# Kernel optimization log

Hardware: AMD Instinct MI355X
Metric: run time of the kernel (lower is better)

## Reference

```python
import jax, jax.numpy as jnp
import numpy as np

N_PRED = 10000
N_GT = 1000
NUM_CLASSES = 80
IMG_H = 800
IMG_W = 1333
EPS = 1e-12
ALPHA, GAMMA, CLS_W = 0.25, 2.0, 2.0
L1_W, IOU_W = 5.0, 2.0
CENTER_RADIUS = 2.5
CAND_TOPK = 5


def _make_boxes(key, n, w, h):
    k1, k2 = jax.random.split(key)
    cxcy = jax.random.uniform(k1, (n, 2)) * jnp.array([w, h], jnp.float32)
    wh = jax.random.uniform(k2, (n, 2)) * 190.0 + 10.0
    return jnp.concatenate([cxcy - wh / 2, cxcy + wh / 2], axis=1).astype(jnp.float32)


def setup_inputs() -> dict:
    key = jax.random.key(0)
    k1, k2, k3, k4 = jax.random.split(key, 4)
    return {
        'pred_logits': jax.random.normal(k1, (N_PRED, NUM_CLASSES), jnp.float32),
        'pred_boxes': _make_boxes(k2, N_PRED, IMG_W, IMG_H),
        'gt_bboxes': _make_boxes(k3, N_GT, IMG_W, IMG_H),
        'gt_labels': jax.random.randint(k4, (N_GT,), 0, NUM_CLASSES),
        'img_h': IMG_H,
        'img_w': IMG_W,
    }


def _pairwise_iou_giou(pred, gt):
    area_p = (pred[:, 2] - pred[:, 0]) * (pred[:, 3] - pred[:, 1])
    area_g = (gt[:, 2] - gt[:, 0]) * (gt[:, 3] - gt[:, 1])
    lt = jnp.maximum(pred[:, None, :2], gt[None, :, :2])
    rb = jnp.minimum(pred[:, None, 2:], gt[None, :, 2:])
    wh = jnp.clip(rb - lt, 0.0)
    inter = wh[..., 0] * wh[..., 1]                       # [N,G]
    union = area_p[:, None] + area_g[None, :] - inter
    iou = inter / jnp.maximum(union, EPS)
    elt = jnp.minimum(pred[:, None, :2], gt[None, :, :2])
    erb = jnp.maximum(pred[:, None, 2:], gt[None, :, 2:])
    ewh = jnp.clip(erb - elt, 0.0)
    enclose = ewh[..., 0] * ewh[..., 1]
    giou = iou - (enclose - union) / jnp.maximum(enclose, EPS)
    return iou, giou


def _center_info(pred, gt):
    # pred/gt in xyxy; uses pred box centers, strict inequalities as in source
    pcx = (pred[:, 0] + pred[:, 2]) * 0.5
    pcy = (pred[:, 1] + pred[:, 3]) * 0.5
    gx1, gy1, gx2, gy2 = gt[:, 0], gt[:, 1], gt[:, 2], gt[:, 3]
    in_boxes = ((pcx[:, None] > gx1) & (pcx[:, None] < gx2) &
                (pcy[:, None] > gy1) & (pcy[:, None] < gy2))
    gcx, gcy = (gx1 + gx2) * 0.5, (gy1 + gy2) * 0.5
    gw, gh = gx2 - gx1, gy2 - gy1
    r = CENTER_RADIUS
    in_centers = ((pcx[:, None] > gcx - r * gw) & (pcx[:, None] < gcx + r * gw) &
                  (pcy[:, None] > gcy - r * gh) & (pcy[:, None] < gcy + r * gh))
    valid = in_boxes.any(1) | in_centers.any(1)
    return valid, in_boxes & in_centers


def _compute_cost_and_ious(pred_logits, pred_boxes, gt_bboxes, gt_labels, img_h, img_w):
    # FocalLossCost
    p = jax.nn.sigmoid(pred_logits)
    neg = -jnp.log1p(-(p - EPS)) * (1 - ALPHA) * p ** GAMMA
    pos = -jnp.log(p + EPS) * ALPHA * (1 - p) ** GAMMA
    cls_cost = (pos - neg)[:, gt_labels] * CLS_W            # [N,G]
    # BBoxL1Cost (normalized by image size)
    factor = jnp.array([img_w, img_h, img_w, img_h], jnp.float32)
    l1_cost = jnp.sum(jnp.abs(pred_boxes[:, None, :] / factor -
                              gt_bboxes[None, :, :] / factor), -1) * L1_W
    # IoUCost (giou) + pairwise ious for dynamic-k
    ious, giou = _pairwise_iou_giou(pred_boxes, gt_bboxes)
    iou_cost = -giou * IOU_W
    valid_mask, in_boxes_and_center = _center_info(pred_boxes, gt_bboxes)
    cost = cls_cost + l1_cost + iou_cost + jnp.where(in_boxes_and_center, 0.0, 100.0)
    cost = cost + jnp.where(valid_mask, 0.0, 10000.0)[:, None]
    return cost, ious


def _dynamic_k_matching(cost, ious):
    n, g = cost.shape
    k = min(CAND_TOPK, n)
    topk_ious, _ = jax.lax.top_k(ious.T, k)                 # [G,k]
    dynamic_ks = jnp.maximum(topk_ious.sum(1).astype(jnp.int32), 1)
    _, idx = jax.lax.top_k(-cost.T, k)                      # [G,k] smallest costs per gt
    vals = (jnp.arange(k)[None, :] < dynamic_ks[:, None]).astype(cost.dtype)
    cols = jnp.broadcast_to(jnp.arange(g)[:, None], (g, k))
    mm = jnp.zeros_like(cost).at[idx, cols].max(vals)       # scatter 1s per gt column
    # resolve priors matched to >1 gt (note: mask is reused stale inside the loop, as in source)
    prior_mask = mm.sum(1) > 1
    cmin = jnp.argmin(cost, axis=1)
    mm = jnp.where(prior_mask[:, None], jax.nn.one_hot(cmin, g, dtype=cost.dtype), mm)

    def cond(state):
        m, _ = state
        return jnp.any(m.sum(0) == 0)

    def body(state):
        m, c = state
        matched_q = m.sum(1) > 0
        c = c + 100000.0 * matched_q[:, None].astype(c.dtype)
        unmatched = m.sum(0) == 0
        pos = jnp.argmin(c, axis=0)                         # [G]
        oh = jax.nn.one_hot(pos, n, dtype=c.dtype).T        # [N,G]
        m = jnp.where(unmatched[None, :], oh, m)
        cmin2 = jnp.argmin(c, axis=1)
        m_fix = jnp.where(prior_mask[:, None], jax.nn.one_hot(cmin2, g, dtype=c.dtype), m)
        m = jnp.where(jnp.any(m.sum(1) > 1), m_fix, m)
        return (m, c)

    mm, _ = jax.lax.while_loop(cond, body, (mm, cost))
    fg_mask = mm.sum(1) > 0
    matched = jnp.argmax(mm, axis=1).astype(jnp.int32)
    return fg_mask, jnp.where(fg_mask, matched, 0)


def reference(pred_logits, pred_boxes, gt_bboxes, gt_labels, img_h, img_w):
    cost, ious = _compute_cost_and_ious(pred_logits, pred_boxes, gt_bboxes,
                                        gt_labels, img_h, img_w)
    fg_mask, matched_gt = _dynamic_k_matching(cost, ious)
    # dense form: matched_gt[i] valid only where fg_mask[i] (fixed-shape version of
    # the original's compressed matched_gt_inds = mm[fg_mask].argmax(1))
    return fg_mask, matched_gt
```

## Files before the change

### kernel.cpp

```cpp
#include <hip/hip_runtime.h>
#include <cfloat>
#include <cmath>

#define NP 10000
#define NG 1000
#define NC 80
#define LMAX 6
#define NCH 4
#define CHSZ (NP / NCH)
#define WMAIN 39
#define WTAIL 4

#define RI_BIG  0x3fffffff
#define KMAX    0xFFFFFFFFFFFFFFFFull

#define TKEY    0xC248000000000000ull

#define WCAP    768

#define PSLOTS  2560
#define PCAP    2560
#define FCAP    1024

__device__ __forceinline__ bool lexless(float av, int ai, float bv, int bi) {
    return (av < bv) || (av == bv && ai < bi);
}

__device__ __forceinline__ unsigned long long packkey(float v, int idx) {
    unsigned u = __float_as_uint(v);
    u ^= (unsigned)(((int)u) >> 31) | 0x80000000u;
    return ((unsigned long long)u << 32) | (unsigned)idx;
}
__device__ __forceinline__ int keyidx(unsigned long long k) {
    return (int)(unsigned)(k & 0xFFFFFFFFu);
}

__device__ __forceinline__ float inflate(float c, int k) {
    for (int q = 0; q < k; q++) c += 100000.0f;
    return c;
}

__device__ __forceinline__ void cost_iou(float4 p, float4 pn, float4 pi,
        float4 g, float4 cb, float4 Gn, float ga, float clsv,
        float& cc_out, float& iou_out) {
#pragma clang fp contract(off)
    float wx = fminf(p.z, g.z) - fmaxf(p.x, g.x); wx = fmaxf(wx, 0.0f);
    float wy = fminf(p.w, g.w) - fmaxf(p.y, g.y); wy = fmaxf(wy, 0.0f);
    float inter = wx * wy;
    float uni = pi.z + ga - inter;
    float iou = inter / fmaxf(uni, 1e-12f);
    float ex = fmaxf(p.z, g.z) - fminf(p.x, g.x); ex = fmaxf(ex, 0.0f);
    float ey = fmaxf(p.w, g.w) - fminf(p.y, g.y); ey = fmaxf(ey, 0.0f);
    float enc = ex * ey;
    float giou = iou - (enc - uni) / fmaxf(enc, 1e-12f);
    float l1 = ((fabsf(pn.x - Gn.x) + fabsf(pn.y - Gn.y))
                + fabsf(pn.z - Gn.z)) + fabsf(pn.w - Gn.w);
    float cc = clsv + l1 * 5.0f;
    cc = cc + (-giou * 2.0f);
    bool inb = (pi.x > g.x && pi.x < g.z && pi.y > g.y && pi.y < g.w);
    bool inc = (pi.x > cb.x && pi.x < cb.z && pi.y > cb.y && pi.y < cb.w);
    cc = cc + ((inb && inc) ? 0.0f : 100.0f);
    cc = cc + pi.w;
    cc_out = cc; iou_out = iou;
}

__device__ __forceinline__ void ins5k(unsigned long long* kv,
        unsigned long long key) {
    if (key < kv[4]) {
        kv[4] = key;
#pragma unroll
        for (int t = 4; t > 0; t--)
            if (kv[t] < kv[t-1]) { unsigned long long tv = kv[t]; kv[t] = kv[t-1]; kv[t-1] = tv; }
    }
}
__device__ __forceinline__ void ins5i(float* iv, float iou) {
    if (iou > iv[4]) {
        iv[4] = iou;
#pragma unroll
        for (int t = 4; t > 0; t--)
            if (iv[t] > iv[t-1]) { float tv = iv[t]; iv[t] = iv[t-1]; iv[t-1] = tv; }
    }
}

__device__ __forceinline__ void cswapk(unsigned long long& a,
        unsigned long long& b) {
    unsigned long long lo = (a < b) ? a : b;
    unsigned long long hi = (a < b) ? b : a;
    a = lo; b = hi;
}
__device__ __forceinline__ void sort5k(unsigned long long* a) {
    cswapk(a[0],a[1]); cswapk(a[3],a[4]); cswapk(a[2],a[4]);
    cswapk(a[2],a[3]); cswapk(a[1],a[4]); cswapk(a[0],a[3]);
    cswapk(a[0],a[2]); cswapk(a[1],a[3]); cswapk(a[1],a[2]);
}
__device__ __forceinline__ void cswapi(float& a, float& b) {
    float hi = fmaxf(a, b), lo = fminf(a, b);
    a = hi; b = lo;
}
__device__ __forceinline__ void sort5i(float* a) {
    cswapi(a[0],a[1]); cswapi(a[3],a[4]); cswapi(a[2],a[4]);
    cswapi(a[2],a[3]); cswapi(a[1],a[4]); cswapi(a[0],a[3]);
    cswapi(a[0],a[2]); cswapi(a[1],a[3]); cswapi(a[1],a[2]);
}

__device__ __forceinline__ void wavemerge5(unsigned long long* kv, float* iv) {
#pragma unroll
    for (int d = 1; d < 64; d <<= 1) {
        unsigned long long r0 = __shfl_xor(kv[0], d);
        unsigned long long r1 = __shfl_xor(kv[1], d);
        unsigned long long r2 = __shfl_xor(kv[2], d);
        unsigned long long r3 = __shfl_xor(kv[3], d);
        unsigned long long r4 = __shfl_xor(kv[4], d);
        kv[0] = (kv[0] < r4) ? kv[0] : r4;
        kv[1] = (kv[1] < r3) ? kv[1] : r3;
        kv[2] = (kv[2] < r2) ? kv[2] : r2;
        kv[3] = (kv[3] < r1) ? kv[3] : r1;
        kv[4] = (kv[4] < r0) ? kv[4] : r0;
        sort5k(kv);
        float s0 = __shfl_xor(iv[0], d);
        float s1 = __shfl_xor(iv[1], d);
        float s2 = __shfl_xor(iv[2], d);
        float s3 = __shfl_xor(iv[3], d);
        float s4 = __shfl_xor(iv[4], d);
        iv[0] = fmaxf(iv[0], s4);
        iv[1] = fmaxf(iv[1], s3);
        iv[2] = fmaxf(iv[2], s2);
        iv[3] = fmaxf(iv[3], s1);
        iv[4] = fmaxf(iv[4], s0);
        sort5i(iv);
    }
}

__device__ __forceinline__ void wavered_lex(float& best, int& bi) {
#pragma unroll
    for (int d = 1; d < 64; d <<= 1) {
        float ov = __shfl_xor(best, d);
        int oi = __shfl_xor(bi, d);
        if (lexless(ov, oi, best, bi)) { best = ov; bi = oi; }
    }
}

#define CLS_TI 64
#define PB_CLS0 40
#define PB_G0   197
#define PB_V0   201
#define PB_SORT 2701
__global__ __launch_bounds__(256) void k_prep(const float* __restrict__ logits,
        const float* __restrict__ pb, const float* __restrict__ gb,
        const int* __restrict__ glab,
        const int* __restrict__ imgw, const int* __restrict__ imgh,
        float* __restrict__ clsval, float4* __restrict__ pnorm,
        float4* __restrict__ pinfo, float4* __restrict__ gcb,
        float4* __restrict__ gnm, float* __restrict__ gar,
        int* rowcnt, int* rowfirst, int* rowiter, int* prior, int* priorcol,
        int* colsum, int* scal, int* priorslot, int* gorder)
{
    __shared__ float sl[CLS_TI * (NC + 1)];
    int b = blockIdx.x;
    if (b == PB_SORT) {
        __shared__ int hist[NC];
        __shared__ int basec[NC];
        int tid = threadIdx.x;
        if (tid < NC) hist[tid] = 0;
        __syncthreads();
        for (int j = tid; j < NG; j += 256) atomicAdd(&hist[glab[j]], 1);
        __syncthreads();
        if (tid == 0) {
            int acc = 0;
            for (int c = 0; c < NC; c++) { basec[c] = acc; acc += hist[c]; }
        }
        __syncthreads();
        for (int j = tid; j < NG; j += 256) {
            int pos = atomicAdd(&basec[glab[j]], 1);
            gorder[pos] = j;
        }
        return;
    }
    if (b < PB_CLS0) {
        int i = b * 256 + threadIdx.x;
        if (i < NP) {
            rowcnt[i] = 0; rowfirst[i] = 0x7fffffff; rowiter[i] = RI_BIG;
            prior[i] = 0; priorcol[i] = 0; priorslot[i] = -1;
        }
        if (i < NG) colsum[i] = 0;
        if (i < 32) scal[i] = 0;
    } else if (b < PB_G0) {
        int i0 = (b - PB_CLS0) * CLS_TI;
        bool full = (i0 + CLS_TI) <= NP;
        if (full) {
            const float* src = logits + (size_t)i0 * NC;
            for (int e = threadIdx.x; e < CLS_TI * NC; e += 256) {
                int di = e / NC, c = e - di * NC;
                sl[di * (NC + 1) + c] = src[e];
            }
        } else {
            for (int e = threadIdx.x; e < CLS_TI * NC; e += 256) {
                int di = e / NC, c = e - di * NC;
                int i = i0 + di;
                sl[di * (NC + 1) + c] = (i < NP) ? logits[(size_t)i * NC + c] : 0.0f;
            }
        }
        __syncthreads();
        for (int e = threadIdx.x; e < CLS_TI * NC; e += 256) {
            int c = e >> 6, di = e & 63;
            int i = i0 + di;
            if (i >= NP) continue;
            float x = sl[di * (NC + 1) + c];
            float p = 1.0f / (1.0f + expf(-x));
            float neg = -log1pf(-(p - 1e-12f)) * 0.75f * (p * p);
            float om = 1.0f - p;
            float pos = -logf(p + 1e-12f) * 0.25f * (om * om);
            clsval[(size_t)c * NP + i] = (pos - neg) * 2.0f;
        }
    } else if (b < PB_V0) {
#pragma clang fp contract(off)
        int j = (b - PB_G0) * 256 + threadIdx.x;
        if (j < NG) {
            float fw = (float)imgw[0], fh = (float)imgh[0];
            float4 g = ((const float4*)gb)[j];
            float gcx = (g.x + g.z) * 0.5f, gcy = (g.y + g.w) * 0.5f;
            float gw = g.z - g.x, gh = g.w - g.y;
            float4 cb; cb.x = gcx - 2.5f * gw; cb.y = gcy - 2.5f * gh;
            cb.z = gcx + 2.5f * gw; cb.w = gcy + 2.5f * gh;
            gcb[j] = cb;
            float4 Gn; Gn.x = g.x / fw; Gn.y = g.y / fh; Gn.z = g.z / fw; Gn.w = g.w / fh;
            gnm[j] = Gn;
            gar[j] = (g.z - g.x) * (g.w - g.y);
        }
    } else {
#pragma clang fp contract(off)
        int wave = threadIdx.x >> 6;
        int lane = threadIdx.x & 63;
        int i = (b - PB_V0) * 4 + wave;
        if (i >= NP) return;
        float4 p = ((const float4*)pb)[i];
        float pcx = (p.x + p.z) * 0.5f, pcy = (p.y + p.w) * 0.5f;
        int vb = 0, vc = 0;
        const float4* gb4 = (const float4*)gb;
        for (int jb = 0; jb < NG; jb += 64) {
            int j = jb + lane;
            if (j < NG) {
                float4 g = gb4[j];
                vb |= (pcx > g.x && pcx < g.z && pcy > g.y && pcy < g.w) ? 1 : 0;
                float gcx = (g.x + g.z) * 0.5f, gcy = (g.y + g.w) * 0.5f;
                float gw = g.z - g.x, gh = g.w - g.y;
                vc |= (pcx > gcx - 2.5f * gw && pcx < gcx + 2.5f * gw &&
                       pcy > gcy - 2.5f * gh && pcy < gcy + 2.5f * gh) ? 1 : 0;
            }
            if (__any(vb | vc)) break;
        }
        int any = __any(vb | vc) ? 1 : 0;
        if (lane == 0) {
            float fw = (float)imgw[0], fh = (float)imgh[0];
            float4 pn; pn.x = p.x / fw; pn.y = p.y / fh; pn.z = p.z / fw; pn.w = p.w / fh;
            pnorm[i] = pn;
            float4 pi4; pi4.x = pcx; pi4.y = pcy;
            pi4.z = (p.z - p.x) * (p.w - p.y);
            pi4.w = any ? 0.0f : 10000.0f;
            pinfo[i] = pi4;
        }
    }
}

__global__ __launch_bounds__(256) void k_cost2(
        const float* __restrict__ pb, const float* __restrict__ gb,
        const int* __restrict__ glab, const float* __restrict__ clsval,
        const float4* __restrict__ pnorm, const float4* __restrict__ pinfo,
        const float4* __restrict__ gcb, const float4* __restrict__ gnm,
        const float* __restrict__ gar, const int* __restrict__ gorder,
        int* __restrict__ rowcnt, int* __restrict__ rowfirst,
        int* __restrict__ rowiter, int* __restrict__ top5,
        int* __restrict__ dkarr)
{
    __shared__ int s_list[4 * WCAP];
    __shared__ unsigned long long s_k4[4][5];
    __shared__ float s_iv4[4][5];
    __shared__ int s_redo;

    int bb = blockIdx.x;
    int j = gorder[(bb & 7) * (NG / 8) + (bb >> 3)];
    int tid = threadIdx.x;
    int wid = tid >> 6;
    int ln  = tid & 63;
    float4 g  = ((const float4*)gb)[j];
    float4 cb = gcb[j];
    float4 Gn = gnm[j];
    float  ga = gar[j];
    const float* clscol = clsval + (size_t)glab[j] * NP;
    const float4* pb4 = (const float4*)pb;
    int base_i = wid * CHSZ;

    int wbase = 0;
    for (int k = 0; k <= WMAIN; k++) {
        bool valid = (k < WMAIN) | (ln < WTAIL);
        int i = base_i + ln + k * 64;
        float4 p = pb4[valid ? i : base_i];
        bool o = valid & (p.z > g.x) & (g.z > p.x) & (p.w > g.y) & (g.w > p.y);
        unsigned long long m = __ballot(o ? 1 : 0);
        if (o) {
            int slot = wbase + __popcll(m & ((1ull << ln) - 1ull));
            if (slot < WCAP) s_list[wid * WCAP + slot] = i;
        }
        wbase += __popcll(m);
    }
    int cnt = wbase;
    bool overflow = (cnt > WCAP);

    unsigned long long kv[5]; float iv[5];
#pragma unroll
    for (int t = 0; t < 5; t++) { kv[t] = KMAX; iv[t] = overflow ? -1.0f : 0.0f; }

    if (!overflow) {
        for (int q = ln; q < cnt; q += 64) {
            int i = s_list[wid * WCAP + q];
            float cc, iou;
            cost_iou(pb4[i], pnorm[i], pinfo[i], g, cb, Gn, ga, clscol[i], cc, iou);
            ins5k(kv, packkey(cc, i)); ins5i(iv, iou);
        }
    } else {
        for (int k = 0; k <= WMAIN; k++) {
            bool valid = (k < WMAIN) | (ln < WTAIL);
            if (valid) {
                int i = base_i + ln + k * 64;
                float cc, iou;
                cost_iou(pb4[i], pnorm[i], pinfo[i], g, cb, Gn, ga, clscol[i], cc, iou);
                ins5k(kv, packkey(cc, i)); ins5i(iv, iou);
            }
        }
    }
    wavemerge5(kv, iv);

    if (ln == 0) {
#pragma unroll
        for (int t = 0; t < 5; t++) { s_k4[wid][t] = kv[t]; s_iv4[wid][t] = iv[t]; }
    }
    __syncthreads();

    unsigned long long mk0=KMAX, mk1=KMAX, mk2=KMAX, mk3=KMAX, mk4=KMAX;
    float mi0=-2.0f, mi1=-2.0f, mi2=-2.0f, mi3=-2.0f, mi4=-2.0f;
    if (tid == 0) {
        int h0 = 0, h1 = 0, h2 = 0, h3 = 0;
        unsigned long long mk[5];
#pragma unroll
        for (int r = 0; r < 5; r++) {
            unsigned long long v0 = (h0 < 5) ? s_k4[0][h0] : KMAX;
            unsigned long long v1 = (h1 < 5) ? s_k4[1][h1] : KMAX;
            unsigned long long v2 = (h2 < 5) ? s_k4[2][h2] : KMAX;
            unsigned long long v3 = (h3 < 5) ? s_k4[3][h3] : KMAX;
            unsigned long long best = v0; int sel = 0;
            if (v1 < best) { best = v1; sel = 1; }
            if (v2 < best) { best = v2; sel = 2; }
            if (v3 < best) { best = v3; sel = 3; }
            mk[r] = best;
            h0 += (sel == 0); h1 += (sel == 1); h2 += (sel == 2); h3 += (sel == 3);
        }
        int g0 = 0, g1 = 0, g2 = 0, g3 = 0;
        float mi[5];
#pragma unroll
        for (int r = 0; r < 5; r++) {
            float w0 = (g0 < 5) ? s_iv4[0][g0] : -2.0f;
            float w1 = (g1 < 5) ? s_iv4[1][g1] : -2.0f;
            float w2 = (g2 < 5) ? s_iv4[2][g2] : -2.0f;
            float w3 = (g3 < 5) ? s_iv4[3][g3] : -2.0f;
            float best = w0; int sel = 0;
            if (w1 > best) { best = w1; sel = 1; }
            if (w2 > best) { best = w2; sel = 2; }
            if (w3 > best) { best = w3; sel = 3; }
            mi[r] = best;
            g0 += (sel == 0); g1 += (sel == 1); g2 += (sel == 2); g3 += (sel == 3);
        }
        mk0 = mk[0]; mk1 = mk[1]; mk2 = mk[2]; mk3 = mk[3]; mk4 = mk[4];
        mi0 = mi[0]; mi1 = mi[1]; mi2 = mi[2]; mi3 = mi[3]; mi4 = mi[4];
        s_redo = (mk4 >= TKEY) ? 1 : 0;
    }
    __syncthreads();

    if (s_redo) {
#pragma unroll
        for (int t = 0; t < 5; t++) { kv[t] = KMAX; iv[t] = -1.0f; }
        for (int k = 0; k <= WMAIN; k++) {
            bool valid = (k < WMAIN) | (ln < WTAIL);
            if (valid) {
                int i = base_i + ln + k * 64;
                float cc, iou;
                cost_iou(pb4[i], pnorm[i], pinfo[i], g, cb, Gn, ga, clscol[i], cc, iou);
                ins5k(kv, packkey(cc, i)); ins5i(iv, iou);
            }
        }
        wavemerge5(kv, iv);
        if (ln == 0) {
#pragma unroll
            for (int t = 0; t < 5; t++) { s_k4[wid][t] = kv[t]; s_iv4[wid][t] = iv[t]; }
        }
        __syncthreads();
        if (tid == 0) {
            int h0 = 0, h1 = 0, h2 = 0, h3 = 0;
            unsigned long long mk[5];
#pragma unroll
            for (int r = 0; r < 5; r++) {
                unsigned long long v0 = (h0 < 5) ? s_k4[0][h0] : KMAX;
                unsigned long long v1 = (h1 < 5) ? s_k4[1][h1] : KMAX;
                unsigned long long v2 = (h2 < 5) ? s_k4[2][h2] : KMAX;
                unsigned long long v3 = (h3 < 5) ? s_k4[3][h3] : KMAX;
                unsigned long long best = v0; int sel = 0;
                if (v1 < best) { best = v1; sel = 1; }
                if (v2 < best) { best = v2; sel = 2; }
                if (v3 < best) { best = v3; sel = 3; }
                mk[r] = best;
                h0 += (sel == 0); h1 += (sel == 1); h2 += (sel == 2); h3 += (sel == 3);
            }
            int g0 = 0, g1 = 0, g2 = 0, g3 = 0;
            float mi[5];
#pragma unroll
            for (int r = 0; r < 5; r++) {
                float w0 = (g0 < 5) ? s_iv4[0][g0] : -2.0f;
                float w1 = (g1 < 5) ? s_iv4[1][g1] : -2.0f;
                float w2 = (g2 < 5) ? s_iv4[2][g2] : -2.0f;
                float w3 = (g3 < 5) ? s_iv4[3][g3] : -2.0f;
                float best = w0; int sel = 0;
                if (w1 > best) { best = w1; sel = 1; }
                if (w2 > best) { best = w2; sel = 2; }
                if (w3 > best) { best = w3; sel = 3; }
                mi[r] = best;
                g0 += (sel == 0); g1 += (sel == 1); g2 += (sel == 2); g3 += (sel == 3);
            }
            mk0 = mk[0]; mk1 = mk[1]; mk2 = mk[2]; mk3 = mk[3]; mk4 = mk[4];
            mi0 = mi[0]; mi1 = mi[1]; mi2 = mi[2]; mi3 = mi[3]; mi4 = mi[4];
        }
    }

    if (tid == 0) {
        float s = (((mi0 + mi1) + mi2) + mi3) + mi4;
        int dk = (int)s;
        if (dk < 1) dk = 1;
        dkarr[j] = dk;
        int b0 = keyidx(mk0), b1 = keyidx(mk1), b2 = keyidx(mk2);
        int b3 = keyidx(mk3), b4 = keyidx(mk4);
        top5[j * 5 + 0] = b0; top5[j * 5 + 1] = b1; top5[j * 5 + 2] = b2;
        top5[j * 5 + 3] = b3; top5[j * 5 + 4] = b4;
#pragma unroll
        for (int t = 0; t < 5; t++) {
            int r = (t == 0) ? b0 : (t == 1) ? b1 : (t == 2) ? b2
                  : (t == 3) ? b3 : b4;
            if (t < dk) {
                atomicAdd(&rowcnt[r], 1);
                atomicMin(&rowfirst[r], j);
                atomicMin(&rowiter[r], -1);
            }
        }
    }
}

__global__ __launch_bounds__(256) void k_pfixsurv(const float* __restrict__ pb,
        const float* __restrict__ gb, const int* __restrict__ glab,
        const float* __restrict__ clsval,
        const float4* __restrict__ pnorm, const float4* __restrict__ pinfo,
        const float4* __restrict__ gcb, const float4* __restrict__ gnm,
        const float* __restrict__ gar,
        int* __restrict__ prior, int* __restrict__ priorcol,
        int* __restrict__ colsum,
        const int* __restrict__ rowcnt, const int* __restrict__ top5,
        const int* __restrict__ dkarr,
        int* __restrict__ scal, int* __restrict__ priorslot,
        float* __restrict__ rowcost)
{
    int b = blockIdx.x;
    int tid = threadIdx.x;
    if (b >= 2500) {
        int j = (b - 2500) * 256 + tid;
        if (j >= NG) return;
        int c = 0;
        int dk = dkarr[j];
        for (int t = 0; t < dk; t++) if (rowcnt[top5[j * 5 + t]] == 1) c++;
        if (c) atomicAdd(&colsum[j], c);
        return;
    }
    __shared__ float rv[256]; __shared__ int ri[256];
    __shared__ int s_slot;
    for (int q = 0; q < 4; q++) {
        int row = b * 4 + q;
        if (rowcnt[row] <= 1) continue;
        if (tid == 0) {
            prior[row] = 1;
            int s = atomicAdd(&scal[20], 1);
            int sl = (s < PSLOTS) ? s : -1;
            priorslot[row] = sl;
            s_slot = sl;
        }
        __syncthreads();
        int slot = s_slot;
        float* rc = (slot >= 0) ? (rowcost + (size_t)slot * NG) : nullptr;
        float4 p = ((const float4*)pb)[row];
        float4 pn = pnorm[row];
        float4 pi4 = pinfo[row];
        float best = FLT_MAX; int bj = 0x7fffffff;
        for (int j = tid; j < NG; j += 256) {
            float cc, iou;
            cost_iou(p, pn, pi4, ((const float4*)gb)[j], gcb[j], gnm[j], gar[j],
                     clsval[(size_t)glab[j] * NP + row], cc, iou);
            if (rc) rc[j] = cc;
            if (lexless(cc, j, best, bj)) { best = cc; bj = j; }
        }
        rv[tid] = best; ri[tid] = bj; __syncthreads();
        for (int w = 128; w > 0; w >>= 1) {
            if (tid < w) {
                float ov = rv[tid + w]; int oi = ri[tid + w];
                if (lexless(ov, oi, rv[tid], ri[tid])) { rv[tid] = ov; ri[tid] = oi; }
            }
            __syncthreads();
        }
        if (tid == 0) {
            priorcol[row] = ri[0];
            atomicAdd(&colsum[ri[0]], 1);
        }
        __syncthreads();
    }
}

__global__ __launch_bounds__(1024) void k_dyn(
        const float* __restrict__ pb, const float* __restrict__ gb,
        const int* __restrict__ glab, const float* __restrict__ clsval,
        const float4* __restrict__ pnorm, const float4* __restrict__ pinfo,
        const float4* __restrict__ gcb, const float4* __restrict__ gnm,
        const float* __restrict__ gar,
        const int* __restrict__ top5, int* __restrict__ rowiter,
        int* __restrict__ rowcnt, int* __restrict__ rowfirst,
        int* __restrict__ colsum, const int* __restrict__ prior,
        int* __restrict__ priorcol, const int* __restrict__ priorslot,
        const float* __restrict__ rowcost, int* __restrict__ out)
{
    __shared__ int s_plist[PCAP];
    __shared__ int s_flist[FCAP];
    __shared__ int s_pcnt;
    __shared__ int s_fcnt;
    __shared__ int s_body;
    __shared__ int s_multi;

    int tid = threadIdx.x;
    int wid = tid >> 6;
    int ln  = tid & 63;
    const float4* pb4 = (const float4*)pb;

    if (tid == 0) { s_pcnt = 0; s_multi = 0; }
    __syncthreads();
    for (int i = tid; i < NP; i += 1024) {
        if (prior[i]) {
            int s = atomicAdd(&s_pcnt, 1);
            if (s < PCAP) s_plist[s] = i;
        }
    }
    __syncthreads();
    int pcnt = (s_pcnt < PCAP) ? s_pcnt : PCAP;

    for (int t = 0; t < LMAX; t++) {
        if (tid == 0) { s_body = 0; s_fcnt = 0; }
        __threadfence();
        __syncthreads();

        for (int j = tid; j < NG; j += 1024) {
            if (colsum[j] != 0) continue;
            s_body = 1;
            int pos = -1;
            for (int r = 0; r < 5; r++) {
                int i = top5[j * 5 + r];
                if (rowiter[i] >= t) { pos = i; break; }
            }
            if (pos < 0) {
                int f = atomicAdd(&s_fcnt, 1);
                if (f < FCAP) s_flist[f] = j;
                continue;
            }
            colsum[j] = 1;
            int old = atomicAdd(&rowcnt[pos], 1);
            if (old >= 1) s_multi = 1;
            atomicMin(&rowfirst[pos], j);
            atomicMin(&rowiter[pos], t);
        }
        __threadfence();
        __syncthreads();

        int fcnt = (s_fcnt < FCAP) ? s_fcnt : FCAP;
        for (int q = wid; q < fcnt; q += 16) {
            int j = s_flist[q];
            float4 g  = ((const float4*)gb)[j];
            float4 cb = gcb[j];
            float4 Gn = gnm[j];
            float  ga = gar[j];
            const float* clscol = clsval + (size_t)glab[j] * NP;
            float best = FLT_MAX; int bi = 0x7fffffff;
            for (int i = ln; i < NP; i += 64) {
                if (rowiter[i] < t) continue;
                float cc, iou;
                cost_iou(pb4[i], pnorm[i], pinfo[i], g, cb, Gn, ga, clscol[i], cc, iou);
                if (lexless(cc, i, best, bi)) { best = cc; bi = i; }
            }
            wavered_lex(best, bi);
            if (ln == 0) {
                colsum[j] = 1;
                int old = atomicAdd(&rowcnt[bi], 1);
                if (old >= 1) s_multi = 1;
                atomicMin(&rowfirst[bi], j);
                atomicMin(&rowiter[bi], t);
            }
        }
        __threadfence();
        __syncthreads();

        if (!s_body) break;

        if (s_multi) {
            for (int q = wid; q < pcnt; q += 16) {
                int row = s_plist[q];
                int k = t - rowiter[row]; if (k < 0) k = 0;
                int slot = priorslot[row];
                float best = FLT_MAX; int bj = 0x7fffffff;
                if (slot >= 0) {
                    const float* rc = rowcost + (size_t)slot * NG;
                    for (int j = ln; j < NG; j += 64) {
                        float val = inflate(rc[j], k);
                        if (lexless(val, j, best, bj)) { best = val; bj = j; }
                    }
                } else {
                    float4 p = pb4[row];
                    float4 pn = pnorm[row];
                    float4 pi4 = pinfo[row];
                    for (int j = ln; j < NG; j += 64) {
                        float cc, iou;
                        cost_iou(p, pn, pi4, ((const float4*)gb)[j], gcb[j],
                                 gnm[j], gar[j],
                                 clsval[(size_t)glab[j] * NP + row], cc, iou);
                        float val = inflate(cc, k);
                        if (lexless(val, j, best, bj)) { best = val; bj = j; }
                    }
                }
                wavered_lex(best, bj);
                if (ln == 0) {
                    int nb = bj;
                    int oldc = priorcol[row];
                    if (nb != oldc) {
                        atomicSub(&colsum[oldc], 1);
                        atomicAdd(&colsum[nb], 1);
                        priorcol[row] = nb;
                    }
                }
            }
        }
        __threadfence();
        __syncthreads();
    }

    __threadfence();
    __syncthreads();
    for (int i = tid; i < NP; i += 1024) {
        int fg = rowcnt[i] > 0;
        out[i] = fg ? 1 : 0;
        out[NP + i] = fg ? (prior[i] ? priorcol[i] : rowfirst[i]) : 0;
    }
}

extern "C" void kernel_launch(void* const* d_in, const int* in_sizes, int n_in,
                              void* d_out, int out_size, void* d_ws, size_t ws_size,
                              hipStream_t stream)
{
    (void)in_sizes; (void)n_in; (void)out_size; (void)ws_size;
    const float* logits = (const float*)d_in[0];
    const float* pboxes = (const float*)d_in[1];
    const float* gboxes = (const float*)d_in[2];
    const int*   glab   = (const int*)d_in[3];
    const int*   imgh   = (const int*)d_in[4];
    const int*   imgw   = (const int*)d_in[5];
    int* out = (int*)d_out;

    char* w = (char*)d_ws;
    float*  clsval  = (float*)(w);
    float4* pnorm   = (float4*)(w + 3200000);
    float4* pinfo   = (float4*)(w + 3360000);
    float4* gcb     = (float4*)(w + 3520000);
    float4* gnm     = (float4*)(w + 3536000);
    float*  gar     = (float*)(w + 3552000);
    int* rowcnt     = (int*)(w + 3556000);
    int* rowfirst   = (int*)(w + 3596000);
    int* rowiter    = (int*)(w + 3636000);
    int* prior      = (int*)(w + 3676000);
    int* priorcol   = (int*)(w + 3716000);
    int* top5       = (int*)(w + 3756000);
    int* dkarr      = (int*)(w + 3776000);
    int* colsum     = (int*)(w + 3780000);
    int* scal       = (int*)(w + 3784000);
    int* priorslot  = (int*)(w + 3784128);
    int* gorder     = (int*)(w + 3824128);
    float* rowcost  = (float*)(w + 3828128);

    hipLaunchKernelGGL(k_prep, dim3(2702), dim3(256), 0, stream,
                       logits, pboxes, gboxes, glab, imgw, imgh,
                       clsval, pnorm, pinfo, gcb, gnm, gar,
                       rowcnt, rowfirst, rowiter, prior, priorcol, colsum, scal,
                       priorslot, gorder);
    hipLaunchKernelGGL(k_cost2, dim3(NG), dim3(256), 0, stream,
                       pboxes, gboxes, glab, clsval, pnorm, pinfo, gcb, gnm, gar,
                       gorder, rowcnt, rowfirst, rowiter, top5, dkarr);
    hipLaunchKernelGGL(k_pfixsurv, dim3(2504), dim3(256), 0, stream,
                       pboxes, gboxes, glab, clsval, pnorm, pinfo, gcb, gnm, gar,
                       prior, priorcol, colsum, rowcnt, top5, dkarr,
                       scal, priorslot, rowcost);
    hipLaunchKernelGGL(k_dyn, dim3(1), dim3(1024), 0, stream,
                       pboxes, gboxes, glab, clsval, pnorm, pinfo, gcb, gnm, gar,
                       top5, rowiter, rowcnt, rowfirst, colsum, prior,
                       priorcol, priorslot, rowcost, out);
}
```

Measured before the change: 173.4 us.

## Bin predictions into a spatial grid to prune per-GT overlap scans

```diff
diff --git a/kernel.cpp b/kernel.cpp
--- a/kernel.cpp
+++ b/kernel.cpp
@@ -16,7 +16,9 @@
 
 #define TKEY    0xC248000000000000ull
 
-#define WCAP    768
+#define GX 16
+#define GY 10
+#define NCELL (GX * GY)
 
 #define PSLOTS  2560
 #define PCAP    2560
@@ -145,6 +147,7 @@
 #define PB_G0   197
 #define PB_V0   201
 #define PB_SORT 2701
+#define PB_GRID 2702
 __global__ __launch_bounds__(256) void k_prep(const float* __restrict__ logits,
         const float* __restrict__ pb, const float* __restrict__ gb,
         const int* __restrict__ glab,
@@ -153,10 +156,58 @@
         float4* __restrict__ pinfo, float4* __restrict__ gcb,
         float4* __restrict__ gnm, float* __restrict__ gar,
         int* rowcnt, int* rowfirst, int* rowiter, int* prior, int* priorcol,
-        int* colsum, int* scal, int* priorslot, int* gorder)
+        int* colsum, int* scal, int* priorslot, int* gorder,
+        int* __restrict__ iorig, int* __restrict__ cellstart,
+        float* __restrict__ gridp)
 {
     __shared__ float sl[CLS_TI * (NC + 1)];
     int b = blockIdx.x;
+    if (b == PB_GRID) {
+        __shared__ int hist[NCELL];
+        __shared__ int basec[NCELL];
+        __shared__ float shw[256];
+        int tid = threadIdx.x;
+        float cw = (float)imgw[0] / (float)GX;
+        float ch = (float)imgh[0] / (float)GY;
+        for (int c = tid; c < NCELL; c += 256) hist[c] = 0;
+        __syncthreads();
+        float hwm = 0.0f;
+        const float4* pb4 = (const float4*)pb;
+        for (int i = tid; i < NP; i += 256) {
+            float4 p = pb4[i];
+            float pcx = (p.x + p.z) * 0.5f, pcy = (p.y + p.w) * 0.5f;
+            hwm = fmaxf(hwm, fmaxf((p.z - p.x) * 0.5f, (p.w - p.y) * 0.5f));
+            int cx = (int)(pcx / cw); cx = min(max(cx, 0), GX - 1);
+            int cy = (int)(pcy / ch); cy = min(max(cy, 0), GY - 1);
+            atomicAdd(&hist[cy * GX + cx], 1);
+        }
+        shw[tid] = hwm;
+        __syncthreads();
+        for (int w = 128; w > 0; w >>= 1) {
+            if (tid < w) shw[tid] = fmaxf(shw[tid], shw[tid + w]);
+            __syncthreads();
+        }
+        if (tid == 0) {
+            gridp[0] = shw[0];
+            gridp[1] = cw;
+            gridp[2] = ch;
+            int acc = 0;
+            for (int c = 0; c < NCELL; c++) {
+                cellstart[c] = acc; basec[c] = acc; acc += hist[c];
+            }
+            cellstart[NCELL] = acc;
+        }
+        __syncthreads();
+        for (int i = tid; i < NP; i += 256) {
+            float4 p = pb4[i];
+            float pcx = (p.x + p.z) * 0.5f, pcy = (p.y + p.w) * 0.5f;
+            int cx = (int)(pcx / cw); cx = min(max(cx, 0), GX - 1);
+            int cy = (int)(pcy / ch); cy = min(max(cy, 0), GY - 1);
+            int pos = atomicAdd(&basec[cy * GX + cx], 1);
+            iorig[pos] = i;
+        }
+        return;
+    }
     if (b == PB_SORT) {
         __shared__ int hist[NC];
         __shared__ int basec[NC];
@@ -262,17 +313,36 @@
     }
 }
 
+__global__ __launch_bounds__(256) void k_sortcopy(const float* __restrict__ pb,
+        const float4* __restrict__ pnorm, const float4* __restrict__ pinfo,
+        const int* __restrict__ iorig,
+        float4* __restrict__ pbs, float4* __restrict__ pns,
+        float4* __restrict__ pis)
+{
+    int s = blockIdx.x * 256 + threadIdx.x;
+    if (s >= NP) return;
+    int i = iorig[s];
+    pbs[s] = ((const float4*)pb)[i];
+    pns[s] = pnorm[i];
+    pis[s] = pinfo[i];
+}
+
 __global__ __launch_bounds__(256) void k_cost2(
         const float* __restrict__ pb, const float* __restrict__ gb,
         const int* __restrict__ glab, const float* __restrict__ clsval,
         const float4* __restrict__ pnorm, const float4* __restrict__ pinfo,
         const float4* __restrict__ gcb, const float4* __restrict__ gnm,
         const float* __restrict__ gar, const int* __restrict__ gorder,
+        const float4* __restrict__ pbs, const float4* __restrict__ pns,
+        const float4* __restrict__ pis, const int* __restrict__ iorig,
+        const int* __restrict__ cellstart, const float* __restrict__ gridp,
         int* __restrict__ rowcnt, int* __restrict__ rowfirst,
         int* __restrict__ rowiter, int* __restrict__ top5,
         int* __restrict__ dkarr)
 {
-    __shared__ int s_list[4 * WCAP];
+    __shared__ int s_seg[GY + 2];
+    __shared__ int s_pre[GY + 2];
+    __shared__ int s_nrow;
     __shared__ unsigned long long s_k4[4][5];
     __shared__ float s_iv4[4][5];
     __shared__ int s_redo;
@@ -290,42 +360,45 @@
     const float4* pb4 = (const float4*)pb;
     int base_i = wid * CHSZ;
 
-    int wbase = 0;
-    for (int k = 0; k <= WMAIN; k++) {
-        bool valid = (k < WMAIN) | (ln < WTAIL);
-        int i = base_i + ln + k * 64;
-        float4 p = pb4[valid ? i : base_i];
-        bool o = valid & (p.z > g.x) & (g.z > p.x) & (p.w > g.y) & (g.w > p.y);
-        unsigned long long m = __ballot(o ? 1 : 0);
+    if (tid == 0) {
+        float R  = gridp[0];
+        float cw = gridp[1];
+        float ch = gridp[2];
+        int cx0 = (int)floorf((g.x - R) / cw); cx0 = min(max(cx0, 0), GX - 1);
+        int cx1 = (int)floorf((g.z + R) / cw); cx1 = min(max(cx1, 0), GX - 1);
+        int cy0 = (int)floorf((g.y - R) / ch); cy0 = min(max(cy0, 0), GY - 1);
+        int cy1 = (int)floorf((g.w + R) / ch); cy1 = min(max(cy1, 0), GY - 1);
+        int nr = 0, acc = 0;
+        for (int cy = cy0; cy <= cy1; cy++) {
+            int s0 = cellstart[cy * GX + cx0];
+            int s1 = cellstart[cy * GX + cx1 + 1];
+            s_seg[nr] = s0; s_pre[nr] = acc; acc += s1 - s0; nr++;
+        }
+        s_pre[nr] = acc;
+        s_nrow = nr;
+        s_redo = 0;
+    }
+    __syncthreads();
+    int nr = s_nrow;
+    int T = s_pre[nr];
+    int lo = (T * wid) >> 2;
+    int hi = (T * (wid + 1)) >> 2;
+
+    unsigned long long kv[5]; float iv[5];
+#pragma unroll
+    for (int t = 0; t < 5; t++) { kv[t] = KMAX; iv[t] = 0.0f; }
+
+    for (int v = lo + ln; v < hi; v += 64) {
+        int rr = 0;
+        while (s_pre[rr + 1] <= v) rr++;
+        int s = s_seg[rr] + (v - s_pre[rr]);
+        float4 p = pbs[s];
+        bool o = (p.z > g.x) & (g.z > p.x) & (p.w > g.y) & (g.w > p.y);
         if (o) {
-            int slot = wbase + __popcll(m & ((1ull << ln) - 1ull));
-            if (slot < WCAP) s_list[wid * WCAP + slot] = i;
-        }
-        wbase += __popcll(m);
-    }
-    int cnt = wbase;
-    bool overflow = (cnt > WCAP);
-
-    unsigned long long kv[5]; float iv[5];
-#pragma unroll
-    for (int t = 0; t < 5; t++) { kv[t] = KMAX; iv[t] = overflow ? -1.0f : 0.0f; }
-
-    if (!overflow) {
-        for (int q = ln; q < cnt; q += 64) {
-            int i = s_list[wid * WCAP + q];
+            int io = iorig[s];
             float cc, iou;
-            cost_iou(pb4[i], pnorm[i], pinfo[i], g, cb, Gn, ga, clscol[i], cc, iou);
-            ins5k(kv, packkey(cc, i)); ins5i(iv, iou);
-        }
-    } else {
-        for (int k = 0; k <= WMAIN; k++) {
-            bool valid = (k < WMAIN) | (ln < WTAIL);
-            if (valid) {
-                int i = base_i + ln + k * 64;
-                float cc, iou;
-                cost_iou(pb4[i], pnorm[i], pinfo[i], g, cb, Gn, ga, clscol[i], cc, iou);
-                ins5k(kv, packkey(cc, i)); ins5i(iv, iou);
-            }
+            cost_iou(p, pns[s], pis[s], g, cb, Gn, ga, clscol[io], cc, iou);
+            ins5k(kv, packkey(cc, io)); ins5i(iv, iou);
         }
     }
     wavemerge5(kv, iv);
@@ -690,15 +763,24 @@
     int* priorslot  = (int*)(w + 3784128);
     int* gorder     = (int*)(w + 3824128);
     float* rowcost  = (float*)(w + 3828128);
-
-    hipLaunchKernelGGL(k_prep, dim3(2702), dim3(256), 0, stream,
+    float4* pbs     = (float4*)(w + 14068128);
+    float4* pns     = (float4*)(w + 14228128);
+    float4* pis     = (float4*)(w + 14388128);
+    int* iorig      = (int*)(w + 14548128);
+    int* cellstart  = (int*)(w + 14588128);
+    float* gridp    = (float*)(w + 14589152);
+
+    hipLaunchKernelGGL(k_prep, dim3(2703), dim3(256), 0, stream,
                        logits, pboxes, gboxes, glab, imgw, imgh,
                        clsval, pnorm, pinfo, gcb, gnm, gar,
                        rowcnt, rowfirst, rowiter, prior, priorcol, colsum, scal,
-                       priorslot, gorder);
+                       priorslot, gorder, iorig, cellstart, gridp);
+    hipLaunchKernelGGL(k_sortcopy, dim3(40), dim3(256), 0, stream,
+                       pboxes, pnorm, pinfo, iorig, pbs, pns, pis);
     hipLaunchKernelGGL(k_cost2, dim3(NG), dim3(256), 0, stream,
                        pboxes, gboxes, glab, clsval, pnorm, pinfo, gcb, gnm, gar,
-                       gorder, rowcnt, rowfirst, rowiter, top5, dkarr);
+                       gorder, pbs, pns, pis, iorig, cellstart, gridp,
+                       rowcnt, rowfirst, rowiter, top5, dkarr);
     hipLaunchKernelGGL(k_pfixsurv, dim3(2504), dim3(256), 0, stream,
                        pboxes, gboxes, glab, clsval, pnorm, pinfo, gcb, gnm, gar,
                        prior, priorcol, colsum, rowcnt, top5, dkarr,
```

Measured after the change: 190.9 us. +10.1%, slower.
